# Performance work log

Hardware: AMD Instinct MI355X
Metric: run time of the kernel (lower is better)

## Reference

```python
import jax, jax.numpy as jnp
import numpy as np

B, T_PAST, T_FUT, GH, GW = 256, 20, 30, 100, 100
HID = 32  # past_encoder_dim


def gru_cell(x, h, w_ih, w_hh, b_ih, b_hh):
    # torch nn.GRU single-cell math; weights [3H, in], [3H, H]
    gi = x @ w_ih.T + b_ih
    gh = h @ w_hh.T + b_hh
    i_r, i_z, i_n = jnp.split(gi, 3, axis=-1)
    h_r, h_z, h_n = jnp.split(gh, 3, axis=-1)
    r = jax.nn.sigmoid(i_r + h_r)
    zg = jax.nn.sigmoid(i_z + h_z)
    n = jnp.tanh(i_n + r * h_n)
    return (1.0 - zg) * n + zg * h


def bilinear(grid, q):
    # grid [B,H,W,C]; q [B,2], dim 0 -> height, dim 1 -> width (matches torch code)
    Bn, Hh, Ww, C = grid.shape
    fy = jnp.clip(jnp.floor(q[:, 0]), 0.0, Hh - 2).astype(jnp.int32)
    fx = jnp.clip(jnp.floor(q[:, 1]), 0.0, Ww - 2).astype(jnp.int32)
    ay = jnp.clip(q[:, 0] - fy, 0.0, 1.0)[:, None]
    ax = jnp.clip(q[:, 1] - fx, 0.0, 1.0)[:, None]
    b = jnp.arange(Bn)
    tl = grid[b, fy, fx]
    tr = grid[b, fy, fx + 1]
    bl = grid[b, fy + 1, fx]
    br = grid[b, fy + 1, fx + 1]
    top = tl + ax * (tr - tl)
    bot = bl + ax * (br - bl)
    return top + ay * (bot - top)  # [B,C]


def setup_inputs() -> dict:
    key = jax.random.key(0)
    ks = jax.random.split(key, 24)
    s = 0.05
    f32 = jnp.float32
    inp = {
        'z': jax.random.normal(ks[0], (B, T_FUT, 2), f32),
        'player_past': jax.random.uniform(ks[1], (B, T_PAST, 2), f32) * (GH - 10),
        'lidar': jax.random.normal(ks[2], (B, GH, GW, 2), f32),
        'conv0_w': jax.random.normal(ks[3], (2, 2, 2, 32), f32) * s,   # HWIO
        'conv0_b': jnp.zeros((32,), f32),
        'conv1_w': jax.random.normal(ks[4], (2, 2, 32, 32), f32) * s,
        'conv1_b': jnp.zeros((32,), f32),
        'conv2_w': jax.random.normal(ks[5], (2, 2, 32, 32), f32) * s,
        'conv2_b': jnp.zeros((32,), f32),
        'conv3_w': jax.random.normal(ks[6], (2, 2, 32, 32), f32) * s,
        'conv3_b': jnp.zeros((32,), f32),
        'enc_wih': jax.random.normal(ks[7], (3 * HID, 2), f32) * s,
        'enc_whh': jax.random.normal(ks[8], (3 * HID, HID), f32) * s,
        'enc_bih': jnp.zeros((3 * HID,), f32),
        'enc_bhh': jnp.zeros((3 * HID,), f32),
        'dec_wih': jax.random.normal(ks[9], (3 * HID, HID + 2), f32) * s,
        'dec_whh': jax.random.normal(ks[10], (3 * HID, HID), f32) * s,
        'dec_bih': jnp.zeros((3 * HID,), f32),
        'dec_bhh': jnp.zeros((3 * HID,), f32),
        'mlp_w1': jax.random.normal(ks[11], (512, HID), f32) * s,
        'mlp_b1': jnp.zeros((512,), f32),
        'mlp_w2': jax.random.normal(ks[12], (4, 512), f32) * s,
        'mlp_b2': jnp.zeros((4,), f32),
    }
    return inp


def reference(z, player_past, lidar,
              conv0_w, conv0_b, conv1_w, conv1_b, conv2_w, conv2_b, conv3_w, conv3_b,
              enc_wih, enc_whh, enc_bih, enc_bhh,
              dec_wih, dec_whh, dec_bih, dec_bhh,
              mlp_w1, mlp_b1, mlp_w2, mlp_b2):
    # field model: ZeroPad2d((0,1,0,1)) + Conv 2x2 + ReLU, x4 -> same-size NHWC conv
    v = lidar
    for w, b in ((conv0_w, conv0_b), (conv1_w, conv1_b), (conv2_w, conv2_b), (conv3_w, conv3_b)):
        v = jax.nn.relu(jax.lax.conv_general_dilated(
            v, w, (1, 1), [(0, 1), (0, 1)],
            dimension_numbers=('NHWC', 'HWIO', 'NHWC')) + b)
    context_lidar = v  # [B,GH,GW,32]

    # past encoder GRU; last output of single-layer GRU == final hidden
    h0 = jnp.zeros((z.shape[0], HID), z.dtype)
    def enc_step(h, x_t):
        return gru_cell(x_t, h, enc_wih, enc_whh, enc_bih, enc_bhh), None
    h_enc, _ = jax.lax.scan(enc_step, h0, jnp.swapaxes(player_past, 0, 1))

    y_tm2 = player_past[:, -2, :]
    y_tm1 = player_past[:, -1, :]

    def dec_step(carry, z_t):
        h, y1, y2 = carry
        interp_t = bilinear(context_lidar, y1)                 # [B,32]
        x = jnp.concatenate([y1, interp_t], axis=-1)            # [B,34]
        h = gru_cell(x, h, dec_wih, dec_whh, dec_bih, dec_bhh)
        # locscale_mlp: Linear(32,512) -> Linear(512,4) (no ReLU between, per source)
        ls = (h @ mlp_w1.T + mlp_b1) @ mlp_w2.T + mlp_b2
        loc = ls[:, :2]
        scale = jax.nn.softplus(ls[:, 2:])
        y_t = 2.0 * y1 - y2 + loc + scale * z_t                 # verlet + affine sample
        return (h, y_t, y1), (y_t, scale)

    _, (ys, scales) = jax.lax.scan(dec_step, (h_enc, y_tm1, y_tm2), jnp.swapaxes(z, 0, 1))
    y = jnp.swapaxes(ys, 0, 1)          # [B,T,2]
    scales = jnp.swapaxes(scales, 0, 1)  # [B,T,2]
    logabsdet = jnp.sum(jnp.log(jnp.abs(jnp.prod(scales, axis=-2))), axis=-1)  # [B]
    return (y, logabsdet)
```

## Files before the change

kernel.cpp:

```cpp
#include <hip/hip_runtime.h>
#include <math.h>

typedef __attribute__((ext_vector_type(8))) short    short8;
typedef __attribute__((ext_vector_type(4))) float    f32x4;
typedef __attribute__((ext_vector_type(4))) unsigned uint4v;

#define FRAG0 256

__device__ __forceinline__ unsigned short f2bf(float f) {
    unsigned u = __builtin_bit_cast(unsigned, f);
    u = u + 0x7fffu + ((u >> 16) & 1u);
    return (unsigned short)(u >> 16);
}
__device__ __forceinline__ unsigned packRNE(float hi, float lo) {
    return (unsigned)f2bf(lo) | ((unsigned)f2bf(hi) << 16);
}
__device__ __forceinline__ unsigned pack_trunc(float hi, float lo) {
    return __builtin_amdgcn_perm(__builtin_bit_cast(unsigned, hi),
                                 __builtin_bit_cast(unsigned, lo), 0x07060302u);
}
__device__ __forceinline__ float rfl(float x) {
    return __builtin_bit_cast(float, __builtin_amdgcn_readfirstlane(__builtin_bit_cast(int, x)));
}
__device__ __forceinline__ f32x4 mfma16(short8 a, short8 b, f32x4 c) {
    return __builtin_amdgcn_mfma_f32_16x16x32_bf16(a, b, c, 0, 0, 0);
}
__device__ __forceinline__ unsigned bperm(int addr, unsigned v) {
    return (unsigned)__builtin_amdgcn_ds_bpermute(addr, (int)v);
}
__device__ __forceinline__ float swz1f(float v){ return __builtin_bit_cast(float, __builtin_amdgcn_ds_swizzle(__builtin_bit_cast(int, v), 0x041F)); }
__device__ __forceinline__ float swz2f(float v){ return __builtin_bit_cast(float, __builtin_amdgcn_ds_swizzle(__builtin_bit_cast(int, v), 0x081F)); }
__device__ __forceinline__ unsigned swz1u(unsigned v){ return (unsigned)__builtin_amdgcn_ds_swizzle((int)v, 0x041F); }
__device__ __forceinline__ float sigf(float x) { return __builtin_amdgcn_rcpf(1.f + __expf(-x)); }
__device__ __forceinline__ float tanhfast(float x) {
    float e = __expf(2.f * x);
    return 1.f - 2.f * __builtin_amdgcn_rcpf(e + 1.f);
}
__device__ __forceinline__ f32x4 ld4(const float* p) { return *(const f32x4*)p; }

__device__ __forceinline__ void packC(unsigned* P, f32x4 a0, f32x4 a1, bool oob) {
    float r0 = fmaxf(a0[0], 0.f), r1 = fmaxf(a0[1], 0.f), r2 = fmaxf(a0[2], 0.f), r3 = fmaxf(a0[3], 0.f);
    float s0 = fmaxf(a1[0], 0.f), s1 = fmaxf(a1[1], 0.f), s2 = fmaxf(a1[2], 0.f), s3 = fmaxf(a1[3], 0.f);
    P[0] = pack_trunc(r1, r0); P[1] = pack_trunc(r3, r2);
    P[2] = pack_trunc(s1, s0); P[3] = pack_trunc(s3, s2);
    if (oob) { P[0] = 0u; P[1] = 0u; P[2] = 0u; P[3] = 0u; }
}

__global__ __launch_bounds__(256) void r2p2_prep(
    const float* __restrict__ w0, const float* __restrict__ w1,
    const float* __restrict__ w2, const float* __restrict__ w3,
    const float* __restrict__ enc_whh,
    const float* __restrict__ dec_wih, const float* __restrict__ dec_whh,
    const float* __restrict__ mw1, const float* __restrict__ mb1,
    const float* __restrict__ mw2, const float* __restrict__ mb2,
    float* __restrict__ wsf, unsigned* __restrict__ wsu) {
    const int tid = threadIdx.x, bx = blockIdx.x;
    if (bx == 0) {
        int o = tid >> 1, half = tid & 1;
        int j = o >> 5, k = o & 31;
        float acc = 0.f;
        const float* w2r = mw2 + j * 512 + half * 256;
        const float* w1c = mw1 + half * 256 * 32 + k;
#pragma unroll 8
        for (int m = 0; m < 256; ++m) acc = fmaf(w2r[m], w1c[m * 32], acc);
        float part = __shfl_xor(acc, 1, 64);
        if (half == 0) wsf[o] = acc + part;
        if (tid < 8) {
            int oc = tid >> 1, hc = tid & 1;
            float a2 = 0.f;
            const float* w2c = mw2 + oc * 512 + hc * 256;
            const float* b1c = mb1 + hc * 256;
#pragma unroll 8
            for (int m = 0; m < 256; ++m) a2 = fmaf(w2c[m], b1c[m], a2);
            float p2 = __shfl_xor(a2, 1, 64);
            if (hc == 0) wsf[128 + oc] = a2 + p2 + mb2[oc];
        }
        return;
    }
    int base = (bx - 1) * 416;
    for (int c = base + tid; c < base + 416 && c < 2816; c += 256) {
        int f = c >> 6, lane = c & 63;
        int n = lane & 15, q = lane >> 4;
        int pc0 = ((n >> 2) << 3) | (n & 3);
        float v[8];
        if (f < 2) {
            int co = pc0 + f * 4;
#pragma unroll
            for (int j = 0; j < 8; ++j) v[j] = (q == 0) ? w0[j * 32 + co] : 0.f;
        } else if (f < 26) {
            int t = f - 2;
            const float* W = (t < 8) ? w1 : (t < 16) ? w2 : w3;
            t &= 7;
            int mt = t >> 2, ks = t & 3, co = pc0 + mt * 4;
#pragma unroll
            for (int j = 0; j < 8; ++j) v[j] = W[(ks * 32 + q * 8 + j) * 32 + co];
        } else if (f < 32) {
            int t = f - 26, gate = t >> 1, mt = t & 1;
            int row = gate * 32 + pc0 + mt * 4;
#pragma unroll
            for (int j = 0; j < 8; ++j) v[j] = dec_wih[row * 34 + 2 + q * 8 + j];
        } else if (f < 38) {
            int t = f - 32, gate = t >> 1, mt = t & 1;
            int row = gate * 32 + pc0 + mt * 4;
#pragma unroll
            for (int j = 0; j < 8; ++j) v[j] = dec_whh[row * 32 + q * 8 + j];
        } else {
            int t = f - 38, gate = t >> 1, mt = t & 1;
            int row = gate * 32 + pc0 + mt * 4;
#pragma unroll
            for (int j = 0; j < 8; ++j) v[j] = enc_whh[row * 32 + q * 8 + j];
        }
        uint4v u;
        u[0] = packRNE(v[1], v[0]); u[1] = packRNE(v[3], v[2]);
        u[2] = packRNE(v[5], v[4]); u[3] = packRNE(v[7], v[6]);
        *(uint4v*)(wsu + FRAG0 + f * 256 + lane * 4) = u;
    }
}

__global__ __launch_bounds__(256, 1) void r2p2_main(
    const float* __restrict__ z, const float* __restrict__ past, const float* __restrict__ lidar,
    const float* __restrict__ b0, const float* __restrict__ b1,
    const float* __restrict__ b2, const float* __restrict__ b3,
    const float* __restrict__ enc_wih, const float* __restrict__ enc_bih, const float* __restrict__ enc_bhh,
    const float* __restrict__ dec_wih, const float* __restrict__ dec_bih, const float* __restrict__ dec_bhh,
    const float* __restrict__ wsf, const unsigned* __restrict__ wsu,
    float* __restrict__ out) {

    const int tid = threadIdx.x, b = blockIdx.x;
    const int wid = tid >> 6, lane = tid & 63;
    const int n = lane & 15, q = lane >> 4, e = n & 1;

    __shared__ __align__(16) unsigned sLID[104 * 104];
    __shared__ __align__(16) float PASTs[40];
    __shared__ __align__(16) float ZVs[64];

    if (wid != 0) {
        int st = tid - 64;
        if (st < 60) ZVs[st] = z[b * 60 + st];
        for (int i = st; i < 816; i += 192) {
            int idx = (i < 416) ? (10400 + i) : ((((i - 416) >> 2) * 104) + 100 + ((i - 416) & 3));
            sLID[idx] = 0u;
        }
        const float4* lp4 = (const float4*)(lidar + (size_t)b * 20000);
#pragma unroll 4
        for (int i = st; i < 5000; i += 192) {
            int r = (int)(((unsigned)i * 5243u) >> 18);
            int c2 = i - r * 50;
            float4 v = lp4[i];
            int o = r * 104 + 2 * c2;
            sLID[o]     = pack_trunc(v.y, v.x);
            sLID[o + 1] = pack_trunc(v.w, v.z);
        }
        __syncthreads();
        return;
    }

    uint4v FR[44];
#pragma unroll
    for (int f = 0; f < 44; ++f) FR[f] = *(const uint4v*)(wsu + FRAG0 + f * 256 + lane * 4);
#define FRG(f) __builtin_bit_cast(short8, FR[f])

    f32x4 cb0[2], cb1[2], cb2[2], cb3[2], gbR[2], gbZ[2], gbNi[2], gbNh[2];
    f32x4 egR[2], egZ[2], egNh[2];
#pragma unroll
    for (int mt = 0; mt < 2; ++mt) {
        int o = q * 8 + mt * 4;
        cb0[mt] = ld4(b0 + o); cb1[mt] = ld4(b1 + o); cb2[mt] = ld4(b2 + o); cb3[mt] = ld4(b3 + o);
        gbR[mt]  = ld4(dec_bih + o)      + ld4(dec_bhh + o);
        gbZ[mt]  = ld4(dec_bih + 32 + o) + ld4(dec_bhh + 32 + o);
        gbNi[mt] = ld4(dec_bih + 64 + o);
        gbNh[mt] = ld4(dec_bhh + 64 + o);
        egR[mt]  = ld4(enc_bih + o)      + ld4(enc_bhh + o);
        egZ[mt]  = ld4(enc_bih + 32 + o) + ld4(enc_bhh + 32 + o);
        egNh[mt] = ld4(enc_bhh + 64 + o);
    }
    f32x4 ebni = ld4(enc_bih + 64 + q * 8 + e * 4);
    float2 wxr[4], wxz[4], wxn[4], wexr[4], wexz[4], wexn[4];
#pragma unroll
    for (int r = 0; r < 4; ++r) {
        int c = q * 8 + e * 4 + r;
        wxr[r]  = *(const float2*)(dec_wih + c * 34);
        wxz[r]  = *(const float2*)(dec_wih + (32 + c) * 34);
        wxn[r]  = *(const float2*)(dec_wih + (64 + c) * 34);
        wexr[r] = *(const float2*)(enc_wih + c * 2);
        wexz[r] = *(const float2*)(enc_wih + (32 + c) * 2);
        wexn[r] = *(const float2*)(enc_wih + (64 + c) * 2);
    }
    short8 Am = (short8)0;
    if (n < 4) {
#pragma unroll
        for (int j = 0; j < 8; ++j) Am[j] = (short)f2bf(wsf[n * 32 + q * 8 + j]);
    }
    f32x4 mcv = {0.f, 0.f, 0.f, 0.f};
    if (q == 0) mcv = *(const f32x4*)(wsf + 128);

    if (lane < 20) *(float2*)&PASTs[2 * lane] = *(const float2*)(past + b * 40 + 2 * lane);
    float q0 = past[b * 40 + 38], q1 = past[b * 40 + 39];
    float p0 = past[b * 40 + 36], p1 = past[b * 40 + 37];
    asm volatile("s_waitcnt lgkmcnt(0)" ::: "memory");

    float hq[4] = {0.f, 0.f, 0.f, 0.f};
    short8 hfr = (short8)0;
#pragma unroll 1
    for (int t = 0; t < 20; ++t) {
        float2 xp = *(const float2*)&PASTs[2 * t];
        f32x4 gr0 = mfma16(FRG(38), hfr, egR[0]),  gr1 = mfma16(FRG(39), hfr, egR[1]);
        f32x4 gz0 = mfma16(FRG(40), hfr, egZ[0]),  gz1 = mfma16(FRG(41), hfr, egZ[1]);
        f32x4 gh0 = mfma16(FRG(42), hfr, egNh[0]), gh1 = mfma16(FRG(43), hfr, egNh[1]);
        f32x4 grS = e ? gr1 : gr0, gzS = e ? gz1 : gz0, ghS = e ? gh1 : gh0;
        float hn[4];
#pragma unroll
        for (int r = 0; r < 4; ++r) {
            float rp = grS[r] + xp.x * wexr[r].x + xp.y * wexr[r].y;
            float zp = gzS[r] + xp.x * wexz[r].x + xp.y * wexz[r].y;
            float pi = ebni[r] + xp.x * wexn[r].x + xp.y * wexn[r].y;
            float rr = sigf(rp), zz = sigf(zp);
            float tn = tanhfast(fmaf(rr, ghS[r], pi));
            float hv = tn + zz * (hq[r] - tn);
            hq[r] = hv; hn[r] = hv;
        }
        unsigned hu0 = packRNE(hn[1], hn[0]), hu1 = packRNE(hn[3], hn[2]);
        unsigned po0 = swz1u(hu0), po1 = swz1u(hu1);
        uint4v hv4;
        hv4[0] = e ? po0 : hu0; hv4[1] = e ? po1 : hu1;
        hv4[2] = e ? hu0 : po0; hv4[3] = e ? hu1 : po1;
        hfr = __builtin_bit_cast(short8, hv4);
    }

    __syncthreads();

    const int pc0 = ((n >> 2) << 3) | (n & 3); (void)pc0;
    int py0a = n / 5, px0a = n % 5;
    int pe0b = (16 + n < 25) ? 16 + n : 24;
    int py0b = pe0b / 5, px0b = pe0b - py0b * 5;
    int ofs0a[4], ofs0b[4];
#pragma unroll
    for (int tp = 0; tp < 4; ++tp) {
        ofs0a[tp] = (py0a + (tp >> 1)) * 104 + px0a + (tp & 1);
        ofs0b[tp] = (py0b + (tp >> 1)) * 104 + px0b + (tp & 1);
    }
    int py1 = n >> 2, px1 = n & 3;
    int adr1[4], sel1m[4];
#pragma unroll
    for (int ks = 0; ks < 4; ++ks) {
        int p = (py1 + (ks >> 1)) * 5 + px1 + (ks & 1);
        adr1[ks] = (q * 16 + (p & 15)) * 4;
        sel1m[ks] = (p >= 16);
    }
    int pe2 = (n < 9) ? n : 8, py2 = pe2 / 3, px2 = pe2 - py2 * 3;
    int adr2[4];
#pragma unroll
    for (int ks = 0; ks < 4; ++ks) adr2[ks] = (q * 16 + (py2 + (ks >> 1)) * 4 + px2 + (ks & 1)) * 4;
    int pe3 = n & 3, py3 = pe3 >> 1, px3 = pe3 & 1;
    int adr3[4];
#pragma unroll
    for (int ks = 0; ks < 4; ++ks) adr3[ks] = (q * 16 + (py3 + (ks >> 1)) * 3 + px3 + (ks & 1)) * 4;
    const f32x4 zf4 = {0.f, 0.f, 0.f, 0.f};
    float la = 0.f;

#pragma unroll 1
    for (int t = 0; t < 30; ++t) {
        float f0 = fminf(fmaxf(floorf(q0), 0.f), 98.f);
        float f1v = fminf(fmaxf(floorf(q1), 0.f), 98.f);
        int fy = (int)f0, fx = (int)f1v;
        float ay = fminf(fmaxf(q0 - f0, 0.f), 1.f);
        float ax = fminf(fmaxf(q1 - f1v, 0.f), 1.f);
        int base = fy * 104 + fx;
        int limy = 100 - fy, limx = 100 - fx;

        short8 bfa = (short8)0, bfb = (short8)0;
        if (q == 0) {
            uint4v ua, ub;
#pragma unroll
            for (int tp = 0; tp < 4; ++tp) { ua[tp] = sLID[base + ofs0a[tp]]; ub[tp] = sLID[base + ofs0b[tp]]; }
            bfa = __builtin_bit_cast(short8, ua);
            bfb = __builtin_bit_cast(short8, ub);
        }
        f32x4 ca0 = mfma16(FRG(0), bfa, cb0[0]);
        f32x4 ca1 = mfma16(FRG(1), bfa, cb0[1]);
        f32x4 cB0 = mfma16(FRG(0), bfb, cb0[0]);
        f32x4 cB1 = mfma16(FRG(1), bfb, cb0[1]);
        unsigned Pa[4], Pb[4];
        packC(Pa, ca0, ca1, (py0a >= limy) || (px0a >= limx));
        packC(Pb, cB0, cB1, (py0b >= limy) || (px0b >= limx));

        short8 bf1[4];
#pragma unroll
        for (int ks = 0; ks < 4; ++ks) {
            uint4v bu;
#pragma unroll
            for (int u = 0; u < 4; ++u) {
                unsigned va = bperm(adr1[ks], Pa[u]);
                unsigned vb = bperm(adr1[ks], Pb[u]);
                bu[u] = sel1m[ks] ? vb : va;
            }
            bf1[ks] = __builtin_bit_cast(short8, bu);
        }
        {
            f32x4 aA = mfma16(FRG(2), bf1[0], cb1[0]); aA = mfma16(FRG(3), bf1[1], aA);
            f32x4 aB = mfma16(FRG(4), bf1[2], zf4);    aB = mfma16(FRG(5), bf1[3], aB);
            f32x4 bA = mfma16(FRG(6), bf1[0], cb1[1]); bA = mfma16(FRG(7), bf1[1], bA);
            f32x4 bB = mfma16(FRG(8), bf1[2], zf4);    bB = mfma16(FRG(9), bf1[3], bB);
            f32x4 o0 = aA + aB, o1 = bA + bB;
            packC(Pa, o0, o1, (py1 >= limy) || (px1 >= limx));
        }

        short8 bf2v[4];
#pragma unroll
        for (int ks = 0; ks < 4; ++ks) {
            uint4v bu;
#pragma unroll
            for (int u = 0; u < 4; ++u) bu[u] = bperm(adr2[ks], Pa[u]);
            bf2v[ks] = __builtin_bit_cast(short8, bu);
        }
        {
            f32x4 aA = mfma16(FRG(10), bf2v[0], cb2[0]); aA = mfma16(FRG(11), bf2v[1], aA);
            f32x4 aB = mfma16(FRG(12), bf2v[2], zf4);    aB = mfma16(FRG(13), bf2v[3], aB);
            f32x4 bA = mfma16(FRG(14), bf2v[0], cb2[1]); bA = mfma16(FRG(15), bf2v[1], bA);
            f32x4 bB = mfma16(FRG(16), bf2v[2], zf4);    bB = mfma16(FRG(17), bf2v[3], bB);
            f32x4 o0 = aA + aB, o1 = bA + bB;
            packC(Pb, o0, o1, (py2 >= limy) || (px2 >= limx));
        }

        short8 bf3v[4];
#pragma unroll
        for (int ks = 0; ks < 4; ++ks) {
            uint4v bu;
#pragma unroll
            for (int u = 0; u < 4; ++u) bu[u] = bperm(adr3[ks], Pb[u]);
            bf3v[ks] = __builtin_bit_cast(short8, bu);
        }
        short8 xf;
        {
            f32x4 aA = mfma16(FRG(18), bf3v[0], cb3[0]); aA = mfma16(FRG(19), bf3v[1], aA);
            f32x4 aB = mfma16(FRG(20), bf3v[2], zf4);    aB = mfma16(FRG(21), bf3v[3], aB);
            f32x4 bA = mfma16(FRG(22), bf3v[0], cb3[1]); bA = mfma16(FRG(23), bf3v[1], bA);
            f32x4 bB = mfma16(FRG(24), bf3v[2], zf4);    bB = mfma16(FRG(25), bf3v[3], bB);
            f32x4 o0 = aA + aB, o1 = bA + bB;
            float wy = (n & 2) ? ay : 1.f - ay;
            float wx = (n & 1) ? ax : 1.f - ax;
            float w = wy * wx;
            float t0[4], t1[4];
#pragma unroll
            for (int r = 0; r < 4; ++r) { t0[r] = fmaxf(o0[r], 0.f) * w; t1[r] = fmaxf(o1[r], 0.f) * w; }
#pragma unroll
            for (int r = 0; r < 4; ++r) { t0[r] += swz1f(t0[r]); t1[r] += swz1f(t1[r]); }
#pragma unroll
            for (int r = 0; r < 4; ++r) { t0[r] += swz2f(t0[r]); t1[r] += swz2f(t1[r]); }
            uint4v xu;
            xu[0] = packRNE(t0[1], t0[0]); xu[1] = packRNE(t0[3], t0[2]);
            xu[2] = packRNE(t1[1], t1[0]); xu[3] = packRNE(t1[3], t1[2]);
            xf = __builtin_bit_cast(short8, xu);
        }

        f32x4 gr0 = mfma16(FRG(26), xf, gbR[0]); gr0 = mfma16(FRG(32), hfr, gr0);
        f32x4 gr1 = mfma16(FRG(27), xf, gbR[1]); gr1 = mfma16(FRG(33), hfr, gr1);
        f32x4 gz0 = mfma16(FRG(28), xf, gbZ[0]); gz0 = mfma16(FRG(34), hfr, gz0);
        f32x4 gz1 = mfma16(FRG(29), xf, gbZ[1]); gz1 = mfma16(FRG(35), hfr, gz1);
        f32x4 gi0 = mfma16(FRG(30), xf, gbNi[0]);
        f32x4 gi1 = mfma16(FRG(31), xf, gbNi[1]);
        f32x4 gh0 = mfma16(FRG(36), hfr, gbNh[0]);
        f32x4 gh1 = mfma16(FRG(37), hfr, gbNh[1]);
        f32x4 grS = e ? gr1 : gr0, gzS = e ? gz1 : gz0, giS = e ? gi1 : gi0, ghS = e ? gh1 : gh0;
        float hn[4];
#pragma unroll
        for (int r = 0; r < 4; ++r) {
            float rp = grS[r] + q0 * wxr[r].x + q1 * wxr[r].y;
            float zp = gzS[r] + q0 * wxz[r].x + q1 * wxz[r].y;
            float pi = giS[r] + q0 * wxn[r].x + q1 * wxn[r].y;
            float rr = sigf(rp), zz = sigf(zp);
            float tn = tanhfast(fmaf(rr, ghS[r], pi));
            float hv = tn + zz * (hq[r] - tn);
            hq[r] = hv; hn[r] = hv;
        }
        unsigned hu0 = packRNE(hn[1], hn[0]), hu1 = packRNE(hn[3], hn[2]);
        unsigned po0 = swz1u(hu0), po1 = swz1u(hu1);
        uint4v hv4;
        hv4[0] = e ? po0 : hu0; hv4[1] = e ? po1 : hu1;
        hv4[2] = e ? hu0 : po0; hv4[3] = e ? hu1 : po1;
        hfr = __builtin_bit_cast(short8, hv4);

        f32x4 ls = mfma16(Am, hfr, mcv);
        float l2 = ls[2], l3 = ls[3];
        float s0 = fmaxf(l2, 0.f) + __logf(1.f + __expf(-fabsf(l2)));
        float s1 = fmaxf(l3, 0.f) + __logf(1.f + __expf(-fabsf(l3)));
        float2 zv = *(const float2*)&ZVs[2 * t];
        float ny0 = 2.f * q0 - p0 + ls[0] + s0 * zv.x;
        float ny1 = 2.f * q1 - p1 + ls[1] + s1 * zv.y;
        if (lane == 0) {
            float2 o2 = {ny0, ny1};
            *(float2*)(out + b * 60 + 2 * t) = o2;
        }
        la += __logf(s0 * s1);
        p0 = q0; p1 = q1;
        q0 = rfl(ny0); q1 = rfl(ny1);
    }
    if (lane == 0) out[15360 + b] = la;
#undef FRG
}

extern "C" void kernel_launch(void* const* d_in, const int* in_sizes, int n_in,
                              void* d_out, int out_size, void* d_ws, size_t ws_size,
                              hipStream_t stream) {
    const float* z    = (const float*)d_in[0];
    const float* past = (const float*)d_in[1];
    const float* lid  = (const float*)d_in[2];
    const float* c0w = (const float*)d_in[3];  const float* c0b = (const float*)d_in[4];
    const float* c1w = (const float*)d_in[5];  const float* c1b = (const float*)d_in[6];
    const float* c2w = (const float*)d_in[7];  const float* c2b = (const float*)d_in[8];
    const float* c3w = (const float*)d_in[9];  const float* c3b = (const float*)d_in[10];
    const float* ewih = (const float*)d_in[11]; const float* ewhh = (const float*)d_in[12];
    const float* ebih = (const float*)d_in[13]; const float* ebhh = (const float*)d_in[14];
    const float* dwih = (const float*)d_in[15]; const float* dwhh = (const float*)d_in[16];
    const float* dbih = (const float*)d_in[17]; const float* dbhh = (const float*)d_in[18];
    const float* mw1 = (const float*)d_in[19]; const float* mb1 = (const float*)d_in[20];
    const float* mw2 = (const float*)d_in[21]; const float* mb2 = (const float*)d_in[22];
    float* out = (float*)d_out;
    float* wsf = (float*)d_ws;
    unsigned* wsu = (unsigned*)d_ws;

    r2p2_prep<<<8, 256, 0, stream>>>(c0w, c1w, c2w, c3w, ewhh, dwih, dwhh,
                                     mw1, mb1, mw2, mb2, wsf, wsu);
    r2p2_main<<<256, 256, 0, stream>>>(z, past, lid, c0b, c1b, c2b, c3b,
                                       ewih, ebih, ebhh, dwih, dbih, dbhh,
                                       wsf, wsu, out);
}
```

Measured before the change: 188.8 us.

## Flatten lane reduction, restructure MLP weight fold, hoist z load, drop occupancy hint

```diff
diff --git a/kernel.cpp b/kernel.cpp
--- a/kernel.cpp
+++ b/kernel.cpp
@@ -28,8 +28,10 @@
 __device__ __forceinline__ unsigned bperm(int addr, unsigned v) {
     return (unsigned)__builtin_amdgcn_ds_bpermute(addr, (int)v);
 }
-__device__ __forceinline__ float swz1f(float v){ return __builtin_bit_cast(float, __builtin_amdgcn_ds_swizzle(__builtin_bit_cast(int, v), 0x041F)); }
-__device__ __forceinline__ float swz2f(float v){ return __builtin_bit_cast(float, __builtin_amdgcn_ds_swizzle(__builtin_bit_cast(int, v), 0x081F)); }
+template<int PAT>
+__device__ __forceinline__ float swzXf(float v) {
+    return __builtin_bit_cast(float, __builtin_amdgcn_ds_swizzle(__builtin_bit_cast(int, v), PAT));
+}
 __device__ __forceinline__ unsigned swz1u(unsigned v){ return (unsigned)__builtin_amdgcn_ds_swizzle((int)v, 0x041F); }
 __device__ __forceinline__ float sigf(float x) { return __builtin_amdgcn_rcpf(1.f + __expf(-x)); }
 __device__ __forceinline__ float tanhfast(float x) {
@@ -56,24 +58,35 @@
     float* __restrict__ wsf, unsigned* __restrict__ wsu) {
     const int tid = threadIdx.x, bx = blockIdx.x;
     if (bx == 0) {
-        int o = tid >> 1, half = tid & 1;
-        int j = o >> 5, k = o & 31;
-        float acc = 0.f;
-        const float* w2r = mw2 + j * 512 + half * 256;
-        const float* w1c = mw1 + half * 256 * 32 + k;
+        __shared__ float red[64];
+        if (tid < 128) {
+            int k = tid & 31, j = tid >> 5;
+            const float* w2r = mw2 + j * 512;
+            float a0 = 0.f, a1 = 0.f, a2 = 0.f, a3 = 0.f;
+#pragma unroll 4
+            for (int m = 0; m < 512; m += 4) {
+                a0 = fmaf(w2r[m],     mw1[m * 32 + k],       a0);
+                a1 = fmaf(w2r[m + 1], mw1[(m + 1) * 32 + k], a1);
+                a2 = fmaf(w2r[m + 2], mw1[(m + 2) * 32 + k], a2);
+                a3 = fmaf(w2r[m + 3], mw1[(m + 3) * 32 + k], a3);
+            }
+            wsf[j * 32 + k] = (a0 + a1) + (a2 + a3);
+        } else if (tid < 192) {
+            int t = tid - 128;
+            int j = t & 3, ch = t >> 2;
+            const float* w2c = mw2 + j * 512 + ch * 32;
+            const float* b1c = mb1 + ch * 32;
+            float p = 0.f;
 #pragma unroll 8
-        for (int m = 0; m < 256; ++m) acc = fmaf(w2r[m], w1c[m * 32], acc);
-        float part = __shfl_xor(acc, 1, 64);
-        if (half == 0) wsf[o] = acc + part;
-        if (tid < 8) {
-            int oc = tid >> 1, hc = tid & 1;
-            float a2 = 0.f;
-            const float* w2c = mw2 + oc * 512 + hc * 256;
-            const float* b1c = mb1 + hc * 256;
-#pragma unroll 8
-            for (int m = 0; m < 256; ++m) a2 = fmaf(w2c[m], b1c[m], a2);
-            float p2 = __shfl_xor(a2, 1, 64);
-            if (hc == 0) wsf[128 + oc] = a2 + p2 + mb2[oc];
+            for (int m = 0; m < 32; ++m) p = fmaf(w2c[m], b1c[m], p);
+            red[t] = p;
+        }
+        __syncthreads();
+        if (tid < 4) {
+            float c = mb2[tid];
+#pragma unroll
+            for (int i = 0; i < 16; ++i) c += red[tid + i * 4];
+            wsf[128 + tid] = c;
         }
         return;
     }
@@ -117,7 +130,8 @@
     }
 }
 
-__global__ __launch_bounds__(256, 1) void r2p2_main(
+__global__ __launch_bounds__(256)
+void r2p2_main(
     const float* __restrict__ z, const float* __restrict__ past, const float* __restrict__ lidar,
     const float* __restrict__ b0, const float* __restrict__ b1,
     const float* __restrict__ b2, const float* __restrict__ b3,
@@ -229,7 +243,6 @@
 
     __syncthreads();
 
-    const int pc0 = ((n >> 2) << 3) | (n & 3); (void)pc0;
     int py0a = n / 5, px0a = n % 5;
     int pe0b = (16 + n < 25) ? 16 + n : 24;
     int py0b = pe0b / 5, px0b = pe0b - py0b * 5;
@@ -260,6 +273,7 @@
 
 #pragma unroll 1
     for (int t = 0; t < 30; ++t) {
+        float2 zv = *(const float2*)&ZVs[2 * t];
         float f0 = fminf(fmaxf(floorf(q0), 0.f), 98.f);
         float f1v = fminf(fmaxf(floorf(q1), 0.f), 98.f);
         int fy = (int)f0, fx = (int)f1v;
@@ -344,9 +358,12 @@
 #pragma unroll
             for (int r = 0; r < 4; ++r) { t0[r] = fmaxf(o0[r], 0.f) * w; t1[r] = fmaxf(o1[r], 0.f) * w; }
 #pragma unroll
-            for (int r = 0; r < 4; ++r) { t0[r] += swz1f(t0[r]); t1[r] += swz1f(t1[r]); }
-#pragma unroll
-            for (int r = 0; r < 4; ++r) { t0[r] += swz2f(t0[r]); t1[r] += swz2f(t1[r]); }
+            for (int r = 0; r < 4; ++r) {
+                float a1 = swzXf<0x041F>(t0[r]), a2 = swzXf<0x081F>(t0[r]), a3 = swzXf<0x0C1F>(t0[r]);
+                t0[r] = (t0[r] + a1) + (a2 + a3);
+                float b1v = swzXf<0x041F>(t1[r]), b2v = swzXf<0x081F>(t1[r]), b3v = swzXf<0x0C1F>(t1[r]);
+                t1[r] = (t1[r] + b1v) + (b2v + b3v);
+            }
             uint4v xu;
             xu[0] = packRNE(t0[1], t0[0]); xu[1] = packRNE(t0[3], t0[2]);
             xu[2] = packRNE(t1[1], t1[0]); xu[3] = packRNE(t1[3], t1[2]);
@@ -384,7 +401,6 @@
         float l2 = ls[2], l3 = ls[3];
         float s0 = fmaxf(l2, 0.f) + __logf(1.f + __expf(-fabsf(l2)));
         float s1 = fmaxf(l3, 0.f) + __logf(1.f + __expf(-fabsf(l3)));
-        float2 zv = *(const float2*)&ZVs[2 * t];
         float ny0 = 2.f * q0 - p0 + ls[0] + s0 * zv.x;
         float ny1 = 2.f * q1 - p1 + ls[1] + s1 * zv.y;
         if (lane == 0) {
```

Result: faster. 182.4 us, median of 2 (-3.4%).
